# Kernel optimization log

Hardware: AMD Instinct MI355X
Metric: run time of the kernel (lower is better)

## Reference

```python
import jax, jax.numpy as jnp
import numpy as np

B, T, N_EMBS, HEAD = 8, 2048, 1024, 64


def setup_inputs() -> dict:
    key = jax.random.key(0)
    k1, k2, k3, k4 = jax.random.split(key, 4)
    x = jax.random.normal(k1, (B, T, N_EMBS), dtype=jnp.float32)
    # nn.Linear(n_embs, head_size, bias=False): y = x @ W^T with W [head, n_embs].
    # We store the transposed weight [n_embs, head] directly for clean einsum.
    s = 1.0 / np.sqrt(N_EMBS)
    Wk = jax.random.uniform(k2, (N_EMBS, HEAD), jnp.float32, -s, s)
    Wq = jax.random.uniform(k3, (N_EMBS, HEAD), jnp.float32, -s, s)
    Wv = jax.random.uniform(k4, (N_EMBS, HEAD), jnp.float32, -s, s)
    return {"x": x, "Wk": Wk, "Wq": Wq, "Wv": Wv}


def reference(x, Wk, Wq, Wv):
    # Single causal self-attention head (dropout rate = 0.0).
    k = jnp.einsum("btn,nh->bth", x, Wk)  # [B,T,H]
    q = jnp.einsum("btn,nh->bth", x, Wq)
    v = jnp.einsum("btn,nh->bth", x, Wv)
    scale = k.shape[-1] ** -0.5
    scores = jnp.einsum("bqh,bkh->bqk", q, k) * scale  # [B,T,T]
    t = x.shape[1]
    causal = jnp.tril(jnp.ones((t, t), dtype=bool))
    scores = jnp.where(causal, scores, -jnp.inf)
    attn = jax.nn.softmax(scores, axis=-1)
    return jnp.einsum("bqk,bkh->bqh", attn, v)  # [B,T,H]
```

## Files before the change

kernel.cpp:

```cpp
#include <hip/hip_runtime.h>
#include <math.h>

#define BB 8
#define TT 2048
#define NE 1024
#define HH 64
#define BT (BB * TT)

typedef __attribute__((ext_vector_type(8))) short s8v;
typedef __attribute__((ext_vector_type(4))) float f4v;

__device__ inline unsigned short f2bf(float f) {
  union { float f; unsigned u; } v;
  v.f = f;
  unsigned r = (v.u + 0x7FFFu + ((v.u >> 16) & 1u)) >> 16;
  return (unsigned short)r;
}

__device__ inline unsigned short f2bf_trunc(float f) {
  union { float f; unsigned u; } v;
  v.f = f;
  return (unsigned short)(v.u >> 16);
}

__device__ inline unsigned cvtpk(float lo, float hi) {
  unsigned r;
  asm("v_cvt_pk_bf16_f32 %0, %1, %2" : "=v"(r) : "v"(lo), "v"(hi));
  return r;
}

__device__ inline void glds16(const unsigned short* g, unsigned short* l) {
  __builtin_amdgcn_global_load_lds(
      (const __attribute__((address_space(1))) unsigned*)g,
      (__attribute__((address_space(3))) unsigned*)l, 16, 0, 0);
}

__global__ __launch_bounds__(256) void conv_wt_kernel(
    const float* __restrict__ Wq, const float* __restrict__ Wk,
    const float* __restrict__ Wv, unsigned short* __restrict__ WTf) {
  const int idx = blockIdx.x * 256 + threadIdx.x;
  const int cb = idx >> 11;
  const int ks = (idx >> 6) & 31;
  const int lane = idx & 63;
  const int lr = lane & 15, lg = lane >> 4;
  const int col = cb * 16 + lr;
  const int m = col >> 6, h = col & 63;
  const int n0 = ks * 32 + lg * 8;
  const float* W = (m == 0) ? Wq : (m == 1) ? Wk : Wv;
  unsigned short v[8];
#pragma unroll
  for (int j = 0; j < 8; ++j) v[j] = f2bf(W[(size_t)(n0 + j) * HH + h]);
  *reinterpret_cast<uint4*>(WTf + (size_t)idx * 8) =
      *reinterpret_cast<const uint4*>(v);
}

__global__ __launch_bounds__(256, 5) void qkv_proj_mfma(
    const float* __restrict__ x, const unsigned short* __restrict__ WTf,
    unsigned short* __restrict__ Q, unsigned short* __restrict__ K,
    unsigned short* __restrict__ VT) {
  __shared__ __align__(16) unsigned short Bbuf[2][6144];
  __shared__ __align__(16) unsigned short Abuf[3][640];

  const int tid = threadIdx.x;
  const int lane = tid & 63;
  const int w = tid >> 6;
  const int lr = lane & 15, lg = lane >> 4;
  const int row0 = blockIdx.x * 16;

  const int arow = tid >> 4, aunit = tid & 15;
  const float* __restrict__ xsrc = x + (size_t)(row0 + arow) * NE + aunit * 2;

  f4v acc[3];
#pragma unroll
  for (int c = 0; c < 3; ++c) acc[c] = (f4v)0.f;

  float2 La[2];

  auto ISSUE_B = [&](int buf, int t) {
#pragma unroll
    for (int j = 0; j < 3; ++j) {
      const int cb = w * 3 + j;
      glds16(WTf + (size_t)(cb * 32 + t) * 512 + lane * 8, &Bbuf[buf][cb * 512]);
    }
  };

  La[0] = *reinterpret_cast<const float2*>(xsrc);
  La[1] = *reinterpret_cast<const float2*>(xsrc + 32);
  ISSUE_B(0, 0);
  *reinterpret_cast<unsigned*>(&Abuf[0][arow * 40 + aunit * 2]) =
      cvtpk(La[0].x, La[0].y);
  La[0] = *reinterpret_cast<const float2*>(xsrc + 2 * 32);
  *reinterpret_cast<unsigned*>(&Abuf[1][arow * 40 + aunit * 2]) =
      cvtpk(La[1].x, La[1].y);
  asm volatile("s_waitcnt vmcnt(1) lgkmcnt(0)" ::: "memory");
  __builtin_amdgcn_s_barrier();
  __builtin_amdgcn_sched_barrier(0);

#pragma unroll
  for (int t = 0; t < 32; ++t) {
    const int cur = t & 1;
    if (t + 1 < 32) ISSUE_B(cur ^ 1, t + 1);
    __builtin_amdgcn_sched_barrier(0);
    if (t + 3 < 32)
      La[(t + 3) & 1] = *reinterpret_cast<const float2*>(xsrc + (t + 3) * 32);
    __builtin_amdgcn_sched_barrier(0);
    const s8v a = *reinterpret_cast<const s8v*>(&Abuf[t % 3][lr * 40 + lg * 8]);
#pragma unroll
    for (int j = 0; j < 3; ++j) {
      const int cb = w * 3 + j;
      const s8v b = *reinterpret_cast<const s8v*>(&Bbuf[cur][cb * 512 + lane * 8]);
      acc[j] = __builtin_amdgcn_mfma_f32_16x16x32_bf16(a, b, acc[j], 0, 0, 0);
    }
    if (t + 2 < 32)
      *reinterpret_cast<unsigned*>(&Abuf[(t + 2) % 3][arow * 40 + aunit * 2]) =
          cvtpk(La[t & 1].x, La[t & 1].y);
    if (t + 1 < 32) {
      if (t + 3 < 32) {
        asm volatile("s_waitcnt vmcnt(1) lgkmcnt(0)" ::: "memory");
      } else {
        asm volatile("s_waitcnt vmcnt(0) lgkmcnt(0)" ::: "memory");
      }
      __builtin_amdgcn_s_barrier();
      __builtin_amdgcn_sched_barrier(0);
    }
  }

  const float QSCL = 0.18033688011112042f;
#pragma unroll
  for (int c = 0; c < 3; ++c) {
    const int col = (w * 3 + c) * 16 + lr;
    const int m = col >> 6;
    const int h = col & 63;
#pragma unroll
    for (int r = 0; r < 4; ++r) {
      const int rr = row0 + lg * 4 + r;
      if (m == 0) {
        Q[(size_t)rr * HH + h] = f2bf(acc[c][r] * QSCL);
      } else if (m == 1) {
        K[(size_t)rr * HH + h] = f2bf(acc[c][r]);
      } else {
        const int bb2 = rr >> 11, tt2 = rr & (TT - 1);
        VT[((size_t)bb2 * HH + h) * TT + tt2] = f2bf(acc[c][r]);
      }
    }
  }
}

__global__ __launch_bounds__(256, 4) void flash_attn_mfma(
    const unsigned short* __restrict__ Q, const unsigned short* __restrict__ K,
    const unsigned short* __restrict__ VT, float* __restrict__ out) {
  __shared__ unsigned short pl[4][16][72];
  __shared__ float ol[4][16][64];
  __shared__ float ml[4][16];
  __shared__ float ll[4][16];

  const int tid = threadIdx.x;
  const int lane = tid & 63;
  const int w = tid >> 6;
  const int lr = lane & 15;
  const int lg = lane >> 4;
  const int bid = blockIdx.x;
  const int b = bid & 7;
  const int qt = 127 - (bid >> 3);
  const int q0 = qt * 16;
  const size_t rowbase = (size_t)b * TT;

  const int nt = (qt >> 2) + 1;
  const int base = nt >> 2, rem = nt & 3;
  const int t0 = w * base + (w < rem ? w : rem);
  const int cnt = base + (w < rem ? 1 : 0);

  const s8v qf0 = *reinterpret_cast<const s8v*>(
      Q + (rowbase + q0 + lr) * HH + lg * 8);
  const s8v qf1 = *reinterpret_cast<const s8v*>(
      Q + (rowbase + q0 + lr) * HH + 32 + lg * 8);

  f4v o[4];
#pragma unroll
  for (int n = 0; n < 4; ++n) o[n] = (f4v)0.f;
  float mrow[4], lrow[4];
#pragma unroll
  for (int r = 0; r < 4; ++r) { mrow[r] = -INFINITY; lrow[r] = 0.f; }

  for (int kt = t0; kt < t0 + cnt; ++kt) {
    const int k0 = kt * 64;
    f4v s[4];
#pragma unroll
    for (int nk = 0; nk < 4; ++nk) s[nk] = (f4v)0.f;
    __builtin_amdgcn_s_setprio(1);
#pragma unroll
    for (int nk = 0; nk < 4; ++nk) {
      const unsigned short* kp = K + (rowbase + k0 + 16 * nk + lr) * HH + lg * 8;
      const s8v kf0 = *reinterpret_cast<const s8v*>(kp);
      const s8v kf1 = *reinterpret_cast<const s8v*>(kp + 32);
      s[nk] = __builtin_amdgcn_mfma_f32_16x16x32_bf16(qf0, kf0, s[nk], 0, 0, 0);
      s[nk] = __builtin_amdgcn_mfma_f32_16x16x32_bf16(qf1, kf1, s[nk], 0, 0, 0);
    }
    __builtin_amdgcn_s_setprio(0);
    s8v vfr[2][4];
#pragma unroll
    for (int kh = 0; kh < 2; ++kh)
#pragma unroll
      for (int n = 0; n < 4; ++n)
        vfr[kh][n] = *reinterpret_cast<const s8v*>(
            VT + ((size_t)b * HH + 16 * n + lr) * TT + k0 + kh * 32 + lg * 8);

    if (kt == nt - 1) {
#pragma unroll
      for (int nk = 0; nk < 4; ++nk) {
        const int kk = k0 + 16 * nk + lr;
#pragma unroll
        for (int r = 0; r < 4; ++r) {
          const int qq = q0 + lg * 4 + r;
          if (kk > qq) s[nk][r] = -INFINITY;
        }
      }
    }

    float mx_[4];
    float grow = -INFINITY;
#pragma unroll
    for (int r = 0; r < 4; ++r) {
      float mx = fmaxf(fmaxf(s[0][r], s[1][r]), fmaxf(s[2][r], s[3][r]));
#pragma unroll
      for (int off = 1; off < 16; off <<= 1)
        mx = fmaxf(mx, __shfl_xor(mx, off));
      mx_[r] = mx;
      grow = fmaxf(grow, mx - mrow[r]);
    }
    if (!__all(grow <= 8.f)) {
#pragma unroll
      for (int r = 0; r < 4; ++r) {
        const float mnew = fmaxf(mrow[r], mx_[r]);
        const float scl = exp2f(mrow[r] - mnew);
        mrow[r] = mnew;
        lrow[r] *= scl;
#pragma unroll
        for (int n = 0; n < 4; ++n) o[n][r] *= scl;
      }
    }
#pragma unroll
    for (int r = 0; r < 4; ++r) {
      float rs = 0.f;
#pragma unroll
      for (int nk = 0; nk < 4; ++nk) {
        const float p = exp2f(s[nk][r] - mrow[r]);
        s[nk][r] = p;
        rs += p;
      }
#pragma unroll
      for (int off = 1; off < 16; off <<= 1)
        rs += __shfl_xor(rs, off);
      lrow[r] += rs;
    }
#pragma unroll
    for (int nk = 0; nk < 4; ++nk)
#pragma unroll
      for (int r = 0; r < 4; ++r)
        pl[w][lg * 4 + r][16 * nk + lr] = f2bf_trunc(s[nk][r]);
#pragma unroll
    for (int kh = 0; kh < 2; ++kh) {
      const int pc = kh * 32 + lg * 8;
      const ushort4 plo = *reinterpret_cast<const ushort4*>(&pl[w][lr][pc]);
      const ushort4 phi = *reinterpret_cast<const ushort4*>(&pl[w][lr][pc + 4]);
      s8v pa;
      pa[0] = plo.x; pa[1] = plo.y; pa[2] = plo.z; pa[3] = plo.w;
      pa[4] = phi.x; pa[5] = phi.y; pa[6] = phi.z; pa[7] = phi.w;
      __builtin_amdgcn_s_setprio(1);
#pragma unroll
      for (int n = 0; n < 4; ++n)
        o[n] = __builtin_amdgcn_mfma_f32_16x16x32_bf16(pa, vfr[kh][n], o[n], 0, 0, 0);
      __builtin_amdgcn_s_setprio(0);
    }
  }

#pragma unroll
  for (int n = 0; n < 4; ++n)
#pragma unroll
    for (int r = 0; r < 4; ++r) ol[w][lg * 4 + r][16 * n + lr] = o[n][r];
  if (lr == 0) {
#pragma unroll
    for (int r = 0; r < 4; ++r) {
      ml[w][lg * 4 + r] = mrow[r];
      ll[w][lg * 4 + r] = lrow[r];
    }
  }
  __syncthreads();

  const int row = tid >> 4;
  const int c0 = (tid & 15) * 4;
  float m0 = ml[0][row], m1 = ml[1][row], m2 = ml[2][row], m3 = ml[3][row];
  const float ms = fmaxf(fmaxf(m0, m1), fmaxf(m2, m3));
  const float w0 = exp2f(m0 - ms), w1 = exp2f(m1 - ms);
  const float w2 = exp2f(m2 - ms), w3 = exp2f(m3 - ms);
  const float lsum = w0 * ll[0][row] + w1 * ll[1][row] +
                     w2 * ll[2][row] + w3 * ll[3][row];
  float4 osum;
  osum.x = w0 * ol[0][row][c0 + 0] + w1 * ol[1][row][c0 + 0] +
           w2 * ol[2][row][c0 + 0] + w3 * ol[3][row][c0 + 0];
  osum.y = w0 * ol[0][row][c0 + 1] + w1 * ol[1][row][c0 + 1] +
           w2 * ol[2][row][c0 + 1] + w3 * ol[3][row][c0 + 1];
  osum.z = w0 * ol[0][row][c0 + 2] + w1 * ol[1][row][c0 + 2] +
           w2 * ol[2][row][c0 + 2] + w3 * ol[3][row][c0 + 2];
  osum.w = w0 * ol[0][row][c0 + 3] + w1 * ol[1][row][c0 + 3] +
           w2 * ol[2][row][c0 + 3] + w3 * ol[3][row][c0 + 3];
  const float inv = 1.0f / lsum;
  float4 res;
  res.x = osum.x * inv; res.y = osum.y * inv;
  res.z = osum.z * inv; res.w = osum.w * inv;
  *reinterpret_cast<float4*>(out + (rowbase + q0 + row) * HH + c0) = res;
}

extern "C" void kernel_launch(void* const* d_in, const int* in_sizes, int n_in,
                              void* d_out, int out_size, void* d_ws, size_t ws_size,
                              hipStream_t stream) {
  const float* x  = (const float*)d_in[0];
  const float* Wk = (const float*)d_in[1];
  const float* Wq = (const float*)d_in[2];
  const float* Wv = (const float*)d_in[3];
  float* out = (float*)d_out;

  unsigned short* ws = (unsigned short*)d_ws;
  unsigned short* Q  = ws;
  unsigned short* K  = ws + (size_t)BT * HH;
  unsigned short* VT = ws + 2 * (size_t)BT * HH;
  unsigned short* WT = ws + 3 * (size_t)BT * HH;

  conv_wt_kernel<<<96, 256, 0, stream>>>(Wq, Wk, Wv, WT);
  qkv_proj_mfma<<<1024, 256, 0, stream>>>(x, WT, Q, K, VT);
  flash_attn_mfma<<<1024, 256, 0, stream>>>(Q, K, VT, out);
}
```

Before: 71.30 us.

## Split attention KV range across two blocks and add combine kernel

Each query tile's causal KV range is now split into two halves handled by separate blocks, doubling the grid to 2048. Each block writes an unnormalized bf16 partial output plus row max and sum to workspace, and a new combine kernel merges the halves. The P staging buffer now reuses the ol shared buffer, which cuts LDS use and allows a higher occupancy hint. The split adds an extra launch, global traffic for the partials, and bf16 rounding of the unnormalized output.

```diff
diff --git a/kernel.cpp b/kernel.cpp
--- a/kernel.cpp
+++ b/kernel.cpp
@@ -15,6 +15,12 @@
   v.f = f;
   unsigned r = (v.u + 0x7FFFu + ((v.u >> 16) & 1u)) >> 16;
   return (unsigned short)r;
+}
+
+__device__ inline float bf2f(unsigned short b) {
+  union { unsigned u; float f; } v;
+  v.u = ((unsigned)b) << 16;
+  return v.f;
 }
 
 __device__ inline unsigned short f2bf_trunc(float f) {
@@ -146,10 +152,10 @@
   }
 }
 
-__global__ __launch_bounds__(256, 4) void flash_attn_mfma(
+__global__ __launch_bounds__(256, 8) void flash_attn_mfma(
     const unsigned short* __restrict__ Q, const unsigned short* __restrict__ K,
-    const unsigned short* __restrict__ VT, float* __restrict__ out) {
-  __shared__ unsigned short pl[4][16][72];
+    const unsigned short* __restrict__ VT, unsigned short* __restrict__ OP,
+    float* __restrict__ ML, float* __restrict__ LL) {
   __shared__ float ol[4][16][64];
   __shared__ float ml[4][16];
   __shared__ float ll[4][16];
@@ -161,13 +167,19 @@
   const int lg = lane >> 4;
   const int bid = blockIdx.x;
   const int b = bid & 7;
-  const int qt = 127 - (bid >> 3);
+  const int qt = 127 - ((bid >> 3) & 127);
+  const int half = bid >> 10;
   const int q0 = qt * 16;
   const size_t rowbase = (size_t)b * TT;
 
+  unsigned short* const plw = reinterpret_cast<unsigned short*>(&ol[w][0][0]);
+
   const int nt = (qt >> 2) + 1;
-  const int base = nt >> 2, rem = nt & 3;
-  const int t0 = w * base + (w < rem ? w : rem);
+  const int nh0 = (nt + 1) >> 1;
+  const int myS = half ? nh0 : 0;
+  const int myC = half ? (nt - nh0) : nh0;
+  const int base = myC >> 2, rem = myC & 3;
+  const int t0 = myS + w * base + (w < rem ? w : rem);
   const int cnt = base + (w < rem ? 1 : 0);
 
   const s8v qf0 = *reinterpret_cast<const s8v*>(
@@ -257,12 +269,13 @@
     for (int nk = 0; nk < 4; ++nk)
 #pragma unroll
       for (int r = 0; r < 4; ++r)
-        pl[w][lg * 4 + r][16 * nk + lr] = f2bf_trunc(s[nk][r]);
+        plw[(lg * 4 + r) * 72 + 16 * nk + lr] = f2bf_trunc(s[nk][r]);
 #pragma unroll
     for (int kh = 0; kh < 2; ++kh) {
       const int pc = kh * 32 + lg * 8;
-      const ushort4 plo = *reinterpret_cast<const ushort4*>(&pl[w][lr][pc]);
-      const ushort4 phi = *reinterpret_cast<const ushort4*>(&pl[w][lr][pc + 4]);
+      const ushort4 plo = *reinterpret_cast<const ushort4*>(&plw[lr * 72 + pc]);
+      const ushort4 phi =
+          *reinterpret_cast<const ushort4*>(&plw[lr * 72 + pc + 4]);
       s8v pa;
       pa[0] = plo.x; pa[1] = plo.y; pa[2] = plo.z; pa[3] = plo.w;
       pa[4] = phi.x; pa[5] = phi.y; pa[6] = phi.z; pa[7] = phi.w;
@@ -274,6 +287,7 @@
     }
   }
 
+  __syncthreads();
 #pragma unroll
   for (int n = 0; n < 4; ++n)
 #pragma unroll
@@ -291,8 +305,9 @@
   const int c0 = (tid & 15) * 4;
   float m0 = ml[0][row], m1 = ml[1][row], m2 = ml[2][row], m3 = ml[3][row];
   const float ms = fmaxf(fmaxf(m0, m1), fmaxf(m2, m3));
-  const float w0 = exp2f(m0 - ms), w1 = exp2f(m1 - ms);
-  const float w2 = exp2f(m2 - ms), w3 = exp2f(m3 - ms);
+  const float msafe = (ms < -1e37f) ? 0.0f : ms;
+  const float w0 = exp2f(m0 - msafe), w1 = exp2f(m1 - msafe);
+  const float w2 = exp2f(m2 - msafe), w3 = exp2f(m3 - msafe);
   const float lsum = w0 * ll[0][row] + w1 * ll[1][row] +
                      w2 * ll[2][row] + w3 * ll[3][row];
   float4 osum;
@@ -304,11 +319,37 @@
            w2 * ol[2][row][c0 + 2] + w3 * ol[3][row][c0 + 2];
   osum.w = w0 * ol[0][row][c0 + 3] + w1 * ol[1][row][c0 + 3] +
            w2 * ol[2][row][c0 + 3] + w3 * ol[3][row][c0 + 3];
-  const float inv = 1.0f / lsum;
+  const size_t pr = (size_t)half * BT + rowbase + q0 + row;
+  ushort4 ov;
+  ov.x = f2bf(osum.x); ov.y = f2bf(osum.y);
+  ov.z = f2bf(osum.z); ov.w = f2bf(osum.w);
+  *reinterpret_cast<ushort4*>(OP + pr * HH + c0) = ov;
+  if ((tid & 15) == 0) {
+    ML[pr] = ms;
+    LL[pr] = lsum;
+  }
+}
+
+__global__ __launch_bounds__(256) void attn_combine(
+    const unsigned short* __restrict__ OP, const float* __restrict__ ML,
+    const float* __restrict__ LL, float* __restrict__ out) {
+  const int idx = blockIdx.x * 256 + threadIdx.x;
+  const int r = idx >> 4;
+  const int c0 = (idx & 15) * 4;
+  const float m0 = ML[r], m1 = ML[BT + r];
+  const float l0 = LL[r], l1 = LL[BT + r];
+  const float ms = fmaxf(m0, m1);
+  const float w0 = exp2f(m0 - ms), w1 = exp2f(m1 - ms);
+  const float inv = 1.0f / (w0 * l0 + w1 * l1);
+  const ushort4 a = *reinterpret_cast<const ushort4*>(OP + (size_t)r * HH + c0);
+  const ushort4 bq =
+      *reinterpret_cast<const ushort4*>(OP + ((size_t)BT + r) * HH + c0);
   float4 res;
-  res.x = osum.x * inv; res.y = osum.y * inv;
-  res.z = osum.z * inv; res.w = osum.w * inv;
-  *reinterpret_cast<float4*>(out + (rowbase + q0 + row) * HH + c0) = res;
+  res.x = (w0 * bf2f(a.x) + w1 * bf2f(bq.x)) * inv;
+  res.y = (w0 * bf2f(a.y) + w1 * bf2f(bq.y)) * inv;
+  res.z = (w0 * bf2f(a.z) + w1 * bf2f(bq.z)) * inv;
+  res.w = (w0 * bf2f(a.w) + w1 * bf2f(bq.w)) * inv;
+  *reinterpret_cast<float4*>(out + (size_t)r * HH + c0) = res;
 }
 
 extern "C" void kernel_launch(void* const* d_in, const int* in_sizes, int n_in,
@@ -325,8 +366,12 @@
   unsigned short* K  = ws + (size_t)BT * HH;
   unsigned short* VT = ws + 2 * (size_t)BT * HH;
   unsigned short* WT = ws + 3 * (size_t)BT * HH;
+  unsigned short* OP = WT + 24576 * 8;
+  float* ML = (float*)(OP + 2 * (size_t)BT * HH);
+  float* LL = ML + 2 * (size_t)BT;
 
   conv_wt_kernel<<<96, 256, 0, stream>>>(Wq, Wk, Wv, WT);
   qkv_proj_mfma<<<1024, 256, 0, stream>>>(x, WT, Q, K, VT);
-  flash_attn_mfma<<<1024, 256, 0, stream>>>(Q, K, VT, out);
-}
+  flash_attn_mfma<<<2048, 256, 0, stream>>>(Q, K, VT, OP, ML, LL);
+  attn_combine<<<1024, 256, 0, stream>>>(OP, ML, LL, out);
+}
```

New measurement: 126.8 us. 1.78x slower.

## Process 128-key tiles per iteration and stagger second-half V loads

Applied to the files above, without the earlier changes.

Each wave now handles 128 keys per loop iteration instead of 64, computing eight score fragments. This halves the number of row max/sum shuffle reductions and online-softmax rescale checks per key. The P·V product is split into two 64-key halves that reuse the per-wave LDS buffer, and the V fragments for the second half are loaded after the first half's MFMAs are issued so their latency can overlap. In exchange, register pressure rises, the split of key tiles across the four waves becomes coarser, and the causal diagonal tile wastes more masked work.

```diff
diff --git a/kernel.cpp b/kernel.cpp
--- a/kernel.cpp
+++ b/kernel.cpp
@@ -165,8 +165,8 @@
   const int q0 = qt * 16;
   const size_t rowbase = (size_t)b * TT;
 
-  const int nt = (qt >> 2) + 1;
-  const int base = nt >> 2, rem = nt & 3;
+  const int nkt = (qt >> 3) + 1;
+  const int base = nkt >> 2, rem = nkt & 3;
   const int t0 = w * base + (w < rem ? w : rem);
   const int cnt = base + (w < rem ? 1 : 0);
 
@@ -182,14 +182,16 @@
 #pragma unroll
   for (int r = 0; r < 4; ++r) { mrow[r] = -INFINITY; lrow[r] = 0.f; }
 
+  const unsigned short* const Vb = VT + (size_t)b * HH * TT;
+
   for (int kt = t0; kt < t0 + cnt; ++kt) {
-    const int k0 = kt * 64;
-    f4v s[4];
-#pragma unroll
-    for (int nk = 0; nk < 4; ++nk) s[nk] = (f4v)0.f;
+    const int k0 = kt * 128;
+    f4v s[8];
+#pragma unroll
+    for (int nk = 0; nk < 8; ++nk) s[nk] = (f4v)0.f;
     __builtin_amdgcn_s_setprio(1);
 #pragma unroll
-    for (int nk = 0; nk < 4; ++nk) {
+    for (int nk = 0; nk < 8; ++nk) {
       const unsigned short* kp = K + (rowbase + k0 + 16 * nk + lr) * HH + lg * 8;
       const s8v kf0 = *reinterpret_cast<const s8v*>(kp);
       const s8v kf1 = *reinterpret_cast<const s8v*>(kp + 32);
@@ -197,17 +199,17 @@
       s[nk] = __builtin_amdgcn_mfma_f32_16x16x32_bf16(qf1, kf1, s[nk], 0, 0, 0);
     }
     __builtin_amdgcn_s_setprio(0);
-    s8v vfr[2][4];
+    s8v vfrA[2][4];
 #pragma unroll
     for (int kh = 0; kh < 2; ++kh)
 #pragma unroll
       for (int n = 0; n < 4; ++n)
-        vfr[kh][n] = *reinterpret_cast<const s8v*>(
-            VT + ((size_t)b * HH + 16 * n + lr) * TT + k0 + kh * 32 + lg * 8);
-
-    if (kt == nt - 1) {
-#pragma unroll
-      for (int nk = 0; nk < 4; ++nk) {
+        vfrA[kh][n] = *reinterpret_cast<const s8v*>(
+            Vb + (size_t)(16 * n + lr) * TT + k0 + kh * 32 + lg * 8);
+
+    if (kt == nkt - 1) {
+#pragma unroll
+      for (int nk = 0; nk < 8; ++nk) {
         const int kk = k0 + 16 * nk + lr;
 #pragma unroll
         for (int r = 0; r < 4; ++r) {
@@ -221,7 +223,8 @@
     float grow = -INFINITY;
 #pragma unroll
     for (int r = 0; r < 4; ++r) {
-      float mx = fmaxf(fmaxf(s[0][r], s[1][r]), fmaxf(s[2][r], s[3][r]));
+      float mx = fmaxf(fmaxf(fmaxf(s[0][r], s[1][r]), fmaxf(s[2][r], s[3][r])),
+                       fmaxf(fmaxf(s[4][r], s[5][r]), fmaxf(s[6][r], s[7][r])));
 #pragma unroll
       for (int off = 1; off < 16; off <<= 1)
         mx = fmaxf(mx, __shfl_xor(mx, off));
@@ -243,7 +246,7 @@
     for (int r = 0; r < 4; ++r) {
       float rs = 0.f;
 #pragma unroll
-      for (int nk = 0; nk < 4; ++nk) {
+      for (int nk = 0; nk < 8; ++nk) {
         const float p = exp2f(s[nk][r] - mrow[r]);
         s[nk][r] = p;
         rs += p;
@@ -253,11 +256,50 @@
         rs += __shfl_xor(rs, off);
       lrow[r] += rs;
     }
+
 #pragma unroll
     for (int nk = 0; nk < 4; ++nk)
 #pragma unroll
       for (int r = 0; r < 4; ++r)
         pl[w][lg * 4 + r][16 * nk + lr] = f2bf_trunc(s[nk][r]);
+    s8v vfrB[2][4];
+    {
+      const ushort4 plo = *reinterpret_cast<const ushort4*>(&pl[w][lr][lg * 8]);
+      const ushort4 phi =
+          *reinterpret_cast<const ushort4*>(&pl[w][lr][lg * 8 + 4]);
+      s8v pa;
+      pa[0] = plo.x; pa[1] = plo.y; pa[2] = plo.z; pa[3] = plo.w;
+      pa[4] = phi.x; pa[5] = phi.y; pa[6] = phi.z; pa[7] = phi.w;
+      __builtin_amdgcn_s_setprio(1);
+#pragma unroll
+      for (int n = 0; n < 4; ++n)
+        o[n] = __builtin_amdgcn_mfma_f32_16x16x32_bf16(pa, vfrA[0][n], o[n], 0, 0, 0);
+      __builtin_amdgcn_s_setprio(0);
+#pragma unroll
+      for (int kh = 0; kh < 2; ++kh)
+#pragma unroll
+        for (int n = 0; n < 4; ++n)
+          vfrB[kh][n] = *reinterpret_cast<const s8v*>(
+              Vb + (size_t)(16 * n + lr) * TT + k0 + 64 + kh * 32 + lg * 8);
+      const ushort4 qlo =
+          *reinterpret_cast<const ushort4*>(&pl[w][lr][32 + lg * 8]);
+      const ushort4 qhi =
+          *reinterpret_cast<const ushort4*>(&pl[w][lr][32 + lg * 8 + 4]);
+      s8v pb;
+      pb[0] = qlo.x; pb[1] = qlo.y; pb[2] = qlo.z; pb[3] = qlo.w;
+      pb[4] = qhi.x; pb[5] = qhi.y; pb[6] = qhi.z; pb[7] = qhi.w;
+      __builtin_amdgcn_s_setprio(1);
+#pragma unroll
+      for (int n = 0; n < 4; ++n)
+        o[n] = __builtin_amdgcn_mfma_f32_16x16x32_bf16(pb, vfrA[1][n], o[n], 0, 0, 0);
+      __builtin_amdgcn_s_setprio(0);
+    }
+
+#pragma unroll
+    for (int nk = 0; nk < 4; ++nk)
+#pragma unroll
+      for (int r = 0; r < 4; ++r)
+        pl[w][lg * 4 + r][16 * nk + lr] = f2bf_trunc(s[4 + nk][r]);
 #pragma unroll
     for (int kh = 0; kh < 2; ++kh) {
       const int pc = kh * 32 + lg * 8;
@@ -269,7 +311,7 @@
       __builtin_amdgcn_s_setprio(1);
 #pragma unroll
       for (int n = 0; n < 4; ++n)
-        o[n] = __builtin_amdgcn_mfma_f32_16x16x32_bf16(pa, vfr[kh][n], o[n], 0, 0, 0);
+        o[n] = __builtin_amdgcn_mfma_f32_16x16x32_bf16(pa, vfrB[kh][n], o[n], 0, 0, 0);
       __builtin_amdgcn_s_setprio(0);
     }
   }
```

After: 79.99 us. 1.12x slower.

## Split attention KV range across eight waves per block and alias P scratch into output buffer

Applied to the files above, without the earlier changes.

The flash-attention kernel now launches 512 threads per block, so eight wavefronts each take a slice of the key tiles for a 16-row query tile instead of four. The per-wave P staging buffer is aliased into the output reduction buffer to keep LDS usage down, which needs an extra barrier before the final combine. The cross-wave log-sum-exp merge now loops over eight partials, with each thread writing two columns. This aims to raise parallelism and shorten the serial KV loop for long causal rows, at the cost of more merge work, LDS traffic and a possible occupancy change.

```diff
diff --git a/kernel.cpp b/kernel.cpp
--- a/kernel.cpp
+++ b/kernel.cpp
@@ -146,13 +146,12 @@
   }
 }
 
-__global__ __launch_bounds__(256, 4) void flash_attn_mfma(
+__global__ __launch_bounds__(512, 4) void flash_attn_mfma(
     const unsigned short* __restrict__ Q, const unsigned short* __restrict__ K,
     const unsigned short* __restrict__ VT, float* __restrict__ out) {
-  __shared__ unsigned short pl[4][16][72];
-  __shared__ float ol[4][16][64];
-  __shared__ float ml[4][16];
-  __shared__ float ll[4][16];
+  __shared__ float ol[8][16][64];
+  __shared__ float ml[8][16];
+  __shared__ float ll[8][16];
 
   const int tid = threadIdx.x;
   const int lane = tid & 63;
@@ -165,8 +164,10 @@
   const int q0 = qt * 16;
   const size_t rowbase = (size_t)b * TT;
 
+  unsigned short* const plw = reinterpret_cast<unsigned short*>(&ol[w][0][0]);
+
   const int nt = (qt >> 2) + 1;
-  const int base = nt >> 2, rem = nt & 3;
+  const int base = nt >> 3, rem = nt & 7;
   const int t0 = w * base + (w < rem ? w : rem);
   const int cnt = base + (w < rem ? 1 : 0);
 
@@ -257,12 +258,13 @@
     for (int nk = 0; nk < 4; ++nk)
 #pragma unroll
       for (int r = 0; r < 4; ++r)
-        pl[w][lg * 4 + r][16 * nk + lr] = f2bf_trunc(s[nk][r]);
+        plw[(lg * 4 + r) * 72 + 16 * nk + lr] = f2bf_trunc(s[nk][r]);
 #pragma unroll
     for (int kh = 0; kh < 2; ++kh) {
       const int pc = kh * 32 + lg * 8;
-      const ushort4 plo = *reinterpret_cast<const ushort4*>(&pl[w][lr][pc]);
-      const ushort4 phi = *reinterpret_cast<const ushort4*>(&pl[w][lr][pc + 4]);
+      const ushort4 plo = *reinterpret_cast<const ushort4*>(&plw[lr * 72 + pc]);
+      const ushort4 phi =
+          *reinterpret_cast<const ushort4*>(&plw[lr * 72 + pc + 4]);
       s8v pa;
       pa[0] = plo.x; pa[1] = plo.y; pa[2] = plo.z; pa[3] = plo.w;
       pa[4] = phi.x; pa[5] = phi.y; pa[6] = phi.z; pa[7] = phi.w;
@@ -274,6 +276,7 @@
     }
   }
 
+  __syncthreads();
 #pragma unroll
   for (int n = 0; n < 4; ++n)
 #pragma unroll
@@ -287,28 +290,32 @@
   }
   __syncthreads();
 
-  const int row = tid >> 4;
-  const int c0 = (tid & 15) * 4;
-  float m0 = ml[0][row], m1 = ml[1][row], m2 = ml[2][row], m3 = ml[3][row];
-  const float ms = fmaxf(fmaxf(m0, m1), fmaxf(m2, m3));
-  const float w0 = exp2f(m0 - ms), w1 = exp2f(m1 - ms);
-  const float w2 = exp2f(m2 - ms), w3 = exp2f(m3 - ms);
-  const float lsum = w0 * ll[0][row] + w1 * ll[1][row] +
-                     w2 * ll[2][row] + w3 * ll[3][row];
-  float4 osum;
-  osum.x = w0 * ol[0][row][c0 + 0] + w1 * ol[1][row][c0 + 0] +
-           w2 * ol[2][row][c0 + 0] + w3 * ol[3][row][c0 + 0];
-  osum.y = w0 * ol[0][row][c0 + 1] + w1 * ol[1][row][c0 + 1] +
-           w2 * ol[2][row][c0 + 1] + w3 * ol[3][row][c0 + 1];
-  osum.z = w0 * ol[0][row][c0 + 2] + w1 * ol[1][row][c0 + 2] +
-           w2 * ol[2][row][c0 + 2] + w3 * ol[3][row][c0 + 2];
-  osum.w = w0 * ol[0][row][c0 + 3] + w1 * ol[1][row][c0 + 3] +
-           w2 * ol[2][row][c0 + 3] + w3 * ol[3][row][c0 + 3];
+  const int row = tid >> 5;
+  const int c0 = (tid & 31) * 2;
+  float mw[8];
+#pragma unroll
+  for (int i = 0; i < 8; ++i) mw[i] = ml[i][row];
+  float ms = mw[0];
+#pragma unroll
+  for (int i = 1; i < 8; ++i) ms = fmaxf(ms, mw[i]);
+  float wt[8];
+  float lsum = 0.f;
+#pragma unroll
+  for (int i = 0; i < 8; ++i) {
+    wt[i] = exp2f(mw[i] - ms);
+    lsum += wt[i] * ll[i][row];
+  }
+  float o0 = 0.f, o1 = 0.f;
+#pragma unroll
+  for (int i = 0; i < 8; ++i) {
+    o0 += wt[i] * ol[i][row][c0 + 0];
+    o1 += wt[i] * ol[i][row][c0 + 1];
+  }
   const float inv = 1.0f / lsum;
-  float4 res;
-  res.x = osum.x * inv; res.y = osum.y * inv;
-  res.z = osum.z * inv; res.w = osum.w * inv;
-  *reinterpret_cast<float4*>(out + (rowbase + q0 + row) * HH + c0) = res;
+  float2 res;
+  res.x = o0 * inv;
+  res.y = o1 * inv;
+  *reinterpret_cast<float2*>(out + (rowbase + q0 + row) * HH + c0) = res;
 }
 
 extern "C" void kernel_launch(void* const* d_in, const int* in_sizes, int n_in,
@@ -328,5 +335,5 @@
 
   conv_wt_kernel<<<96, 256, 0, stream>>>(Wq, Wk, Wv, WT);
   qkv_proj_mfma<<<1024, 256, 0, stream>>>(x, WT, Q, K, VT);
-  flash_attn_mfma<<<1024, 256, 0, stream>>>(Q, K, VT, out);
-}
+  flash_attn_mfma<<<1024, 512, 0, stream>>>(Q, K, VT, out);
+}
```

Result: faster. 69.03 us (-3.2%).
